# Performance work log

Measured on AMD Instinct MI355X. Metric: run time of the kernel, lower is better.

Reference implementation:

```python
import jax, jax.numpy as jnp
import numpy as np

QMIN, QMAX = -128, 127


def setup_inputs() -> dict:
    key = jax.random.key(0)
    kx, kw, kb = jax.random.split(key, 3)
    B, S, IN, OUT = 4, 2048, 4096, 4096
    x = jax.random.normal(kx, (B, S, IN), dtype=jnp.float32)
    # int8-valued weight stored as int32 for portability
    weight_int = jax.random.randint(kw, (OUT, IN), QMIN, QMAX + 1, dtype=jnp.int32)
    bias = jax.random.normal(kb, (OUT,), dtype=jnp.float32) * 0.02
    # plausible frozen qparams: x~N(0,1) -> range ~[-4,4]; weight range ~[-3,3] pre-quant
    scale_a = jnp.asarray(8.0 / 255.0, dtype=jnp.float32)
    zp_a = jnp.asarray(0, dtype=jnp.int32)
    weight_scale = jnp.asarray(6.0 / 255.0, dtype=jnp.float32)
    weight_zero_point = jnp.asarray(0, dtype=jnp.int32)
    return {
        "x": x,
        "weight_int": weight_int,
        "bias": bias,
        "scale_a": scale_a,
        "zp_a": zp_a,
        "weight_scale": weight_scale,
        "weight_zero_point": weight_zero_point,
    }


def reference(x, weight_int, bias, scale_a, zp_a, weight_scale, weight_zero_point):
    # fake-quantize activations: round(x/scale)+zp, clamp to int8 range
    zp_a_f = zp_a.astype(jnp.float32)
    x_int8 = jnp.clip(jnp.round(x / scale_a) + zp_a_f, QMIN, QMAX)
    x_cent = x_int8 - zp_a_f                                   # [B,S,IN]
    w_cent = weight_int.astype(jnp.float32) - weight_zero_point.astype(jnp.float32)  # [OUT,IN]
    y = jnp.einsum("bsi,oi->bso", x_cent, w_cent)              # dequant-space GEMM
    y = y * (scale_a * weight_scale)
    y = y + bias
    return y
```

## Files before the change

kernel.cpp:

```cpp
#include <hip/hip_runtime.h>
#include <stdint.h>

typedef int v4i  __attribute__((ext_vector_type(4)));
typedef int v16i __attribute__((ext_vector_type(16)));

__global__ void quant_x_kernel(const float* __restrict__ x,
                               int8_t* __restrict__ xq,
                               int* __restrict__ sum_x,
                               const float* __restrict__ p_scale,
                               const int* __restrict__ p_zp,
                               int K) {
    const int row = blockIdx.x;
    const int t = threadIdx.x;
    const float s = p_scale[0];
    const float zpf = (float)p_zp[0];
    const float* xr = x + (size_t)row * K;
    int8_t* qr = xq + (size_t)row * K;
    int lsum = 0;
    const int nchunk = K >> 10;
    for (int i = 0; i < nchunk; ++i) {
        const int idx = (i << 10) + (t << 2);
        const float4 v = *reinterpret_cast<const float4*>(xr + idx);
        const float f0 = fminf(fmaxf(rintf(v.x / s) + zpf, -128.f), 127.f);
        const float f1 = fminf(fmaxf(rintf(v.y / s) + zpf, -128.f), 127.f);
        const float f2 = fminf(fmaxf(rintf(v.z / s) + zpf, -128.f), 127.f);
        const float f3 = fminf(fmaxf(rintf(v.w / s) + zpf, -128.f), 127.f);
        const int i0 = (int)f0, i1 = (int)f1, i2 = (int)f2, i3 = (int)f3;
        lsum += i0 + i1 + i2 + i3;
        const unsigned pk = (unsigned)(i0 & 255) | ((unsigned)(i1 & 255) << 8) |
                            ((unsigned)(i2 & 255) << 16) | ((unsigned)(i3 & 255) << 24);
        *reinterpret_cast<unsigned*>(qr + idx) = pk;
    }
    __shared__ int wsum[4];
    #pragma unroll
    for (int off = 32; off > 0; off >>= 1) lsum += __shfl_down(lsum, off);
    if ((t & 63) == 0) wsum[t >> 6] = lsum;
    __syncthreads();
    if (t == 0) sum_x[row] = wsum[0] + wsum[1] + wsum[2] + wsum[3];
}

__global__ void quant_w_kernel(const int* __restrict__ w,
                               int8_t* __restrict__ wq,
                               int* __restrict__ sum_w,
                               int K) {
    const int row = blockIdx.x;
    const int t = threadIdx.x;
    const int* wr_ = w + (size_t)row * K;
    int8_t* qr = wq + (size_t)row * K;
    int lsum = 0;
    const int nchunk = K >> 10;
    for (int i = 0; i < nchunk; ++i) {
        const int idx = (i << 10) + (t << 2);
        const int4 v = *reinterpret_cast<const int4*>(wr_ + idx);
        lsum += v.x + v.y + v.z + v.w;
        const unsigned pk = (unsigned)(v.x & 255) | ((unsigned)(v.y & 255) << 8) |
                            ((unsigned)(v.z & 255) << 16) | ((unsigned)(v.w & 255) << 24);
        *reinterpret_cast<unsigned*>(qr + idx) = pk;
    }
    __shared__ int wsum[4];
    #pragma unroll
    for (int off = 32; off > 0; off >>= 1) lsum += __shfl_down(lsum, off);
    if ((t & 63) == 0) wsum[t >> 6] = lsum;
    __syncthreads();
    if (t == 0) sum_w[row] = wsum[0] + wsum[1] + wsum[2] + wsum[3];
}

#define BM 256
#define BN 256
#define BKB 64
#define NSLOT 4

__device__ __forceinline__ void gload_lds16(const void* g, void* l) {
    __builtin_amdgcn_global_load_lds(
        (const __attribute__((address_space(1))) unsigned int*)g,
        (__attribute__((address_space(3))) unsigned int*)l, 16, 0, 0);
}

#define MFMA_I8 __builtin_amdgcn_mfma_i32_32x32x32_i8

__global__ __launch_bounds__(256, 1)
void gemm_i8_kernel(const int8_t* __restrict__ xq,
                    const int8_t* __restrict__ wq,
                    const int* __restrict__ sum_x,
                    const int* __restrict__ sum_w,
                    const float* __restrict__ bias,
                    float* __restrict__ out,
                    const float* __restrict__ p_sa,
                    const int* __restrict__ p_zpa,
                    const float* __restrict__ p_sw,
                    const int* __restrict__ p_wzp,
                    int M, int N, int K) {
    __shared__ v4i ldsA[NSLOT][1024];
    __shared__ v4i ldsB[NSLOT][1024];

    const int tid = threadIdx.x;
    const int lane = tid & 63;
    const int wid = tid >> 6;
    const int wr = wid >> 1;
    const int wc = wid & 1;

    const int nwgy = M / BM;
    const int nwg = nwgy * (N / BN);
    const int bid = blockIdx.x;
    const int v = (bid & 7) * (nwg >> 3) + (bid >> 3);
    const int m0 = (v % nwgy) * BM;
    const int n0 = (v / nwgy) * BN;

    const int srow = tid >> 2;
    const int schunk = (tid & 3) ^ (((srow >> 1) ^ (srow >> 3)) & 3);
    const int8_t* aS = xq + (size_t)(m0 + srow) * K + schunk * 16;
    const int8_t* bS = wq + (size_t)(n0 + srow) * K + schunk * 16;
    const size_t qtr = (size_t)64 * K;
    const int dbase = wid * 64;

    const int sel = ((lane >> 1) ^ (lane >> 3)) & 3;
    const int hi = lane >> 5;
    const int c0 = hi ^ sel;
    const int c1 = (2 + hi) ^ sel;
    int arow[4], brow[4];
    #pragma unroll
    for (int i = 0; i < 4; ++i) {
        arow[i] = (wr * 128 + i * 32 + (lane & 31)) * 4;
        brow[i] = (wc * 128 + i * 32 + (lane & 31)) * 4;
    }

    v16i acc[4][4] = {};
    const int NT = K / BKB;

#define STAGE(SLOT, T_) do {                                                  \
        const int8_t* pa_ = aS + (size_t)(T_) * BKB;                          \
        const int8_t* pb_ = bS + (size_t)(T_) * BKB;                          \
        _Pragma("unroll")                                                     \
        for (int k_ = 0; k_ < 4; ++k_) {                                      \
            gload_lds16(pa_ + k_ * qtr, &ldsA[SLOT][k_ * 256 + dbase]);       \
            gload_lds16(pb_ + k_ * qtr, &ldsB[SLOT][k_ * 256 + dbase]);       \
        }                                                                     \
    } while (0)

    STAGE(0, 0);
    STAGE(1, 1);
    asm volatile("s_waitcnt vmcnt(8)" ::: "memory");
    __builtin_amdgcn_sched_barrier(0);
    __builtin_amdgcn_s_barrier();

    for (int t = 0; t < NT; ++t) {
        const v4i* LA = ldsA[t & 3];
        const v4i* LB = ldsB[t & 3];
        v4i a[4][2], b[4][2];
        #pragma unroll
        for (int i = 0; i < 4; ++i) {
            a[i][0] = LA[arow[i] + c0];
            a[i][1] = LA[arow[i] + c1];
        }
        #pragma unroll
        for (int i = 0; i < 4; ++i) {
            b[i][0] = LB[brow[i] + c0];
            b[i][1] = LB[brow[i] + c1];
        }
        if (t + 2 < NT) STAGE((t + 2) & 3, t + 2);
        __builtin_amdgcn_s_setprio(1);
        #pragma unroll
        for (int ks = 0; ks < 2; ++ks)
            #pragma unroll
            for (int rf = 0; rf < 4; ++rf)
                #pragma unroll
                for (int cf = 0; cf < 4; ++cf)
                    acc[rf][cf] = MFMA_I8(a[rf][ks], b[cf][ks], acc[rf][cf], 0, 0, 0);
        __builtin_amdgcn_s_setprio(0);
        if (t + 2 < NT) {
            asm volatile("s_waitcnt vmcnt(8)" ::: "memory");
        } else if (t + 1 < NT) {
            asm volatile("s_waitcnt vmcnt(0)" ::: "memory");
        }
        __builtin_amdgcn_sched_barrier(0);
        __builtin_amdgcn_s_barrier();
    }
#undef STAGE

    const float stot = p_sa[0] * p_sw[0];
    const int zpa = p_zpa[0];
    const int wzp = p_wzp[0];
    const int kzz = K * zpa * wzp;
    const int coll = lane & 31;
    const int rhi = (lane >> 5) * 4;

    #pragma unroll
    for (int cf = 0; cf < 4; ++cf) {
        const int cg = n0 + wc * 128 + cf * 32 + coll;
        const int sw = sum_w[cg];
        const float bb = bias[cg];
        #pragma unroll
        for (int rf = 0; rf < 4; ++rf) {
            const int rbase = m0 + wr * 128 + rf * 32 + rhi;
            #pragma unroll
            for (int r = 0; r < 16; ++r) {
                const int rowg = rbase + (r & 3) + 8 * (r >> 2);
                const int iv = acc[rf][cf][r] - wzp * sum_x[rowg] - zpa * sw + kzz;
                out[(size_t)rowg * N + cg] = (float)iv * stot + bb;
            }
        }
    }
}

extern "C" void kernel_launch(void* const* d_in, const int* in_sizes, int n_in,
                              void* d_out, int out_size, void* d_ws, size_t ws_size,
                              hipStream_t stream) {
    const float* x     = (const float*)d_in[0];
    const int*   w     = (const int*)d_in[1];
    const float* bias  = (const float*)d_in[2];
    const float* p_sa  = (const float*)d_in[3];
    const int*   p_zpa = (const int*)d_in[4];
    const float* p_sw  = (const float*)d_in[5];
    const int*   p_wzp = (const int*)d_in[6];

    const int N = in_sizes[2];
    const int K = in_sizes[1] / N;
    const int M = in_sizes[0] / K;

    int8_t* xq = (int8_t*)d_ws;
    int8_t* wq = xq + (size_t)M * K;
    int* sum_x = (int*)(wq + (size_t)N * K);
    int* sum_w = sum_x + M;

    quant_x_kernel<<<M, 256, 0, stream>>>(x, xq, sum_x, p_sa, p_zpa, K);
    quant_w_kernel<<<N, 256, 0, stream>>>(w, wq, sum_w, K);

    const int nwg = (M / BM) * (N / BN);
    gemm_i8_kernel<<<nwg, 256, 0, stream>>>(xq, wq, sum_x, sum_w, bias,
                                            (float*)d_out, p_sa, p_zpa, p_sw, p_wzp,
                                            M, N, K);
}
```

Before: 238.4 us.

## Use eight waves per block and stage two K-tiles per pipeline step

The GEMM block grows from 256 to 512 threads, arranged as a 2x4 wave grid, so each wave owns a 128x64 output sub-tile instead of 128x128. This halves the accumulator registers per wave and puts more waves on the MFMA units to hide latency. The main loop now stages and consumes two 64-byte K-tiles per iteration and waits on all outstanding loads (vmcnt(0)) before each barrier. In exchange, each A fragment is read from LDS by four waves instead of two, and the coarser wait removes some of the fine-grained overlap of the old one-tile-ahead schedule.

```diff
diff --git a/kernel.cpp b/kernel.cpp
--- a/kernel.cpp
+++ b/kernel.cpp
@@ -78,7 +78,7 @@
 
 #define MFMA_I8 __builtin_amdgcn_mfma_i32_32x32x32_i8
 
-__global__ __launch_bounds__(256, 1)
+__global__ __launch_bounds__(512, 1)
 void gemm_i8_kernel(const int8_t* __restrict__ xq,
                     const int8_t* __restrict__ wq,
                     const int* __restrict__ sum_x,
@@ -96,8 +96,8 @@
     const int tid = threadIdx.x;
     const int lane = tid & 63;
     const int wid = tid >> 6;
-    const int wr = wid >> 1;
-    const int wc = wid & 1;
+    const int wr = wid >> 2;
+    const int wc = wid & 3;
 
     const int nwgy = M / BM;
     const int nwg = nwgy * (N / BN);
@@ -110,72 +110,74 @@
     const int schunk = (tid & 3) ^ (((srow >> 1) ^ (srow >> 3)) & 3);
     const int8_t* aS = xq + (size_t)(m0 + srow) * K + schunk * 16;
     const int8_t* bS = wq + (size_t)(n0 + srow) * K + schunk * 16;
-    const size_t qtr = (size_t)64 * K;
+    const size_t half = (size_t)128 * K;
     const int dbase = wid * 64;
 
     const int sel = ((lane >> 1) ^ (lane >> 3)) & 3;
     const int hi = lane >> 5;
+    const int abase = (wr * 128 + (lane & 31)) * 4;
+    const int bbase = (wc * 64 + (lane & 31)) * 4;
     const int c0 = hi ^ sel;
     const int c1 = (2 + hi) ^ sel;
-    int arow[4], brow[4];
-    #pragma unroll
-    for (int i = 0; i < 4; ++i) {
-        arow[i] = (wr * 128 + i * 32 + (lane & 31)) * 4;
-        brow[i] = (wc * 128 + i * 32 + (lane & 31)) * 4;
-    }
-
-    v16i acc[4][4] = {};
+
+    v16i acc[4][2] = {};
     const int NT = K / BKB;
 
-#define STAGE(SLOT, T_) do {                                                  \
-        const int8_t* pa_ = aS + (size_t)(T_) * BKB;                          \
-        const int8_t* pb_ = bS + (size_t)(T_) * BKB;                          \
-        _Pragma("unroll")                                                     \
-        for (int k_ = 0; k_ < 4; ++k_) {                                      \
-            gload_lds16(pa_ + k_ * qtr, &ldsA[SLOT][k_ * 256 + dbase]);       \
-            gload_lds16(pb_ + k_ * qtr, &ldsB[SLOT][k_ * 256 + dbase]);       \
-        }                                                                     \
+#define STAGE_TILE(TT) do {                                                   \
+        const int ns_ = (TT) & 3;                                             \
+        const int8_t* pa_ = aS + (size_t)(TT) * BKB;                          \
+        const int8_t* pb_ = bS + (size_t)(TT) * BKB;                          \
+        gload_lds16(pa_,        &ldsA[ns_][dbase]);                           \
+        gload_lds16(pa_ + half, &ldsA[ns_][dbase + 512]);                     \
+        gload_lds16(pb_,        &ldsB[ns_][dbase]);                           \
+        gload_lds16(pb_ + half, &ldsB[ns_][dbase + 512]);                     \
     } while (0)
 
-    STAGE(0, 0);
-    STAGE(1, 1);
-    asm volatile("s_waitcnt vmcnt(8)" ::: "memory");
+    STAGE_TILE(0);
+    STAGE_TILE(1);
+    asm volatile("s_waitcnt vmcnt(0)" ::: "memory");
     __builtin_amdgcn_sched_barrier(0);
     __builtin_amdgcn_s_barrier();
 
-    for (int t = 0; t < NT; ++t) {
-        const v4i* LA = ldsA[t & 3];
-        const v4i* LB = ldsB[t & 3];
-        v4i a[4][2], b[4][2];
+    const int NSEG = NT / 2;
+    for (int s = 0; s < NSEG; ++s) {
+        const int t0 = 2 * s;
+        if (s + 1 < NSEG) {
+            STAGE_TILE(t0 + 2);
+            STAGE_TILE(t0 + 3);
+        }
+        v4i a[2][8], b[2][4];
         #pragma unroll
-        for (int i = 0; i < 4; ++i) {
-            a[i][0] = LA[arow[i] + c0];
-            a[i][1] = LA[arow[i] + c1];
-        }
-        #pragma unroll
-        for (int i = 0; i < 4; ++i) {
-            b[i][0] = LB[brow[i] + c0];
-            b[i][1] = LB[brow[i] + c1];
-        }
-        if (t + 2 < NT) STAGE((t + 2) & 3, t + 2);
+        for (int j = 0; j < 2; ++j) {
+            const v4i* LA = ldsA[(t0 + j) & 3];
+            const v4i* LB = ldsB[(t0 + j) & 3];
+            b[j][0] = LB[bbase + c0];
+            b[j][1] = LB[bbase + c1];
+            b[j][2] = LB[bbase + 128 + c0];
+            b[j][3] = LB[bbase + 128 + c1];
+            #pragma unroll
+            for (int rf = 0; rf < 4; ++rf) {
+                a[j][rf * 2 + 0] = LA[abase + rf * 128 + c0];
+                a[j][rf * 2 + 1] = LA[abase + rf * 128 + c1];
+            }
+        }
         __builtin_amdgcn_s_setprio(1);
         #pragma unroll
-        for (int ks = 0; ks < 2; ++ks)
+        for (int j = 0; j < 2; ++j) {
             #pragma unroll
-            for (int rf = 0; rf < 4; ++rf)
-                #pragma unroll
-                for (int cf = 0; cf < 4; ++cf)
-                    acc[rf][cf] = MFMA_I8(a[rf][ks], b[cf][ks], acc[rf][cf], 0, 0, 0);
+            for (int rf = 0; rf < 4; ++rf) {
+                acc[rf][0] = MFMA_I8(a[j][rf * 2 + 0], b[j][0], acc[rf][0], 0, 0, 0);
+                acc[rf][1] = MFMA_I8(a[j][rf * 2 + 0], b[j][2], acc[rf][1], 0, 0, 0);
+                acc[rf][0] = MFMA_I8(a[j][rf * 2 + 1], b[j][1], acc[rf][0], 0, 0, 0);
+                acc[rf][1] = MFMA_I8(a[j][rf * 2 + 1], b[j][3], acc[rf][1], 0, 0, 0);
+            }
+        }
         __builtin_amdgcn_s_setprio(0);
-        if (t + 2 < NT) {
-            asm volatile("s_waitcnt vmcnt(8)" ::: "memory");
-        } else if (t + 1 < NT) {
-            asm volatile("s_waitcnt vmcnt(0)" ::: "memory");
-        }
+        asm volatile("s_waitcnt vmcnt(0)" ::: "memory");
         __builtin_amdgcn_sched_barrier(0);
         __builtin_amdgcn_s_barrier();
     }
-#undef STAGE
+#undef STAGE_TILE
 
     const float stot = p_sa[0] * p_sw[0];
     const int zpa = p_zpa[0];
@@ -185,8 +187,8 @@
     const int rhi = (lane >> 5) * 4;
 
     #pragma unroll
-    for (int cf = 0; cf < 4; ++cf) {
-        const int cg = n0 + wc * 128 + cf * 32 + coll;
+    for (int cf = 0; cf < 2; ++cf) {
+        const int cg = n0 + wc * 64 + cf * 32 + coll;
         const int sw = sum_w[cg];
         const float bb = bias[cg];
         #pragma unroll
@@ -226,7 +228,7 @@
     quant_w_kernel<<<N, 256, 0, stream>>>(w, wq, sum_w, K);
 
     const int nwg = (M / BM) * (N / BN);
-    gemm_i8_kernel<<<nwg, 256, 0, stream>>>(xq, wq, sum_x, sum_w, bias,
+    gemm_i8_kernel<<<nwg, 512, 0, stream>>>(xq, wq, sum_x, sum_w, bias,
                                             (float*)d_out, p_sa, p_zpa, p_sw, p_wzp,
                                             M, N, K);
 }
```

Result: slower. 244.7 us (+2.7%).
